# Performance work log

Measured on AMD Instinct MI355X. Metric: run time of the kernel, lower is better.

Reference implementation:

```python
import jax, jax.numpy as jnp
import numpy as np

N, E = 50000, 800000
IN_C, HID, OUT_C = 100, 128, 40
LAYERS, GROUPS, CODES = 3, 3, 16
BETA = 0.98
EPS = 1e-5


def setup_inputs() -> dict:
    key = jax.random.key(0)
    ks = jax.random.split(key, 16)
    lin = lambda k, i, o: (jax.random.normal(k, (i, o), jnp.float32) / np.sqrt(i)).astype(jnp.float32)
    d = {}
    d["x"] = jax.random.normal(ks[0], (N, IN_C), jnp.float32)
    d["src"] = jax.random.randint(ks[1], (E,), 0, N, jnp.int32)
    d["dst"] = jax.random.randint(ks[2], (E,), 0, N, jnp.int32)
    # SAGEConv params: lin_l (aggregated, with bias) and lin_r (root, no bias)
    d["W0a"], d["W0r"], d["b0"] = lin(ks[3], IN_C, HID), lin(ks[4], IN_C, HID), jnp.zeros((HID,), jnp.float32)
    d["W1a"], d["W1r"], d["b1"] = lin(ks[5], HID, HID), lin(ks[6], HID, HID), jnp.zeros((HID,), jnp.float32)
    d["W2a"], d["W2r"], d["b2"] = lin(ks[7], HID, HID), lin(ks[8], HID, HID), jnp.zeros((HID,), jnp.float32)
    # BatchNorm (eval mode: running stats) for first num_layers-1 = 2 layers
    d["bn_gamma"] = jnp.ones((2, HID), jnp.float32)
    d["bn_beta"] = jnp.zeros((2, HID), jnp.float32)
    d["bn_mean"] = jnp.zeros((2, HID), jnp.float32)
    d["bn_var"] = jnp.ones((2, HID), jnp.float32)
    # Residual VQ codebooks: [layer, group, num_codes, feature]
    d["codebooks"] = 0.1 * jax.random.normal(ks[9], (LAYERS, GROUPS, CODES, HID), jnp.float32)
    d["lin_W"] = lin(ks[10], HID, OUT_C)
    d["lin_b"] = jnp.zeros((OUT_C,), jnp.float32)
    return d


def _sage_conv(h, src, dst, Wa, Wr, b):
    # mean neighbor aggregation (PyG SAGEConv, aggr='mean')
    msg = h[src]                                              # [E, d]
    agg = jax.ops.segment_sum(msg, dst, num_segments=N)       # [N, d]
    deg = jax.ops.segment_sum(jnp.ones((E,), h.dtype), dst, num_segments=N)
    agg = agg / jnp.maximum(deg, 1.0)[:, None]
    return agg @ Wa + b + h @ Wr


def _rvq(h, cb):
    # residual vector quantization over GROUPS codebooks; cb: [G, K, D]
    res, quant, ids = h, jnp.zeros_like(h), []
    for g in range(GROUPS):
        c = cb[g]                                             # [K, D]
        d2 = (jnp.sum(res * res, -1, keepdims=True)
              - 2.0 * res @ c.T + jnp.sum(c * c, -1))          # [N, K]
        idx = jnp.argmin(d2, axis=-1)
        q = c[idx]
        quant = quant + q
        res = res - q
        ids.append(idx)
    sg = jax.lax.stop_gradient
    loss = (BETA * jnp.mean((h - sg(quant)) ** 2)
            + (1.0 - BETA) * jnp.mean((sg(h) - quant) ** 2))
    return loss, jnp.stack(ids, axis=1)                        # [N, G] int


def reference(x, src, dst, W0a, W0r, b0, W1a, W1r, b1, W2a, W2r, b2,
              bn_gamma, bn_beta, bn_mean, bn_var, codebooks, lin_W, lin_b):
    Ws = [(W0a, W0r, b0), (W1a, W1r, b1), (W2a, W2r, b2)]
    h = x
    total_loss = jnp.float32(0.0)
    id_list = []
    for i in range(LAYERS - 1):
        h = _sage_conv(h, src, dst, *Ws[i])
        h = (h - bn_mean[i]) * jax.lax.rsqrt(bn_var[i] + EPS) * bn_gamma[i] + bn_beta[i]
        h = jax.nn.relu(h)                                     # dropout: eval mode (identity)
        loss, ids = _rvq(h, codebooks[i])
        total_loss = total_loss + loss
        id_list.append(ids)
    h = _sage_conv(h, src, dst, *Ws[-1])
    loss, ids = _rvq(h, codebooks[-1])
    total_loss = total_loss + loss
    id_list.append(ids)
    out = h @ lin_W + lin_b
    return out, total_loss, jnp.concatenate(id_list, axis=1)
```

## Files before the change

kernel.cpp:

```cpp
#include <hip/hip_runtime.h>

#define NN 50000
#define HID 128
#define IN_C 100
#define OUT_C 40

__global__ __launch_bounds__(256)
void hist_kernel(const int* __restrict__ dst, int* __restrict__ deg, int E) {
    int e = blockIdx.x * 256 + threadIdx.x;
    if (e < E) atomicAdd(&deg[dst[e]], 1);
}

__global__ __launch_bounds__(256)
void chunk_sum_kernel(const int* __restrict__ deg, int* __restrict__ chunk_sums, int N) {
    __shared__ int s[256];
    const int t = threadIdx.x;
    const int i = blockIdx.x * 256 + t;
    s[t] = (i < N) ? deg[i] : 0;
    __syncthreads();
    for (int o = 128; o; o >>= 1) { if (t < o) s[t] += s[t + o]; __syncthreads(); }
    if (t == 0) chunk_sums[blockIdx.x] = s[0];
}

__global__ __launch_bounds__(256)
void chunk_scan_kernel(int* __restrict__ chunk_sums, int M) {
    __shared__ int s[256];
    const int t = threadIdx.x;
    int v = (t < M) ? chunk_sums[t] : 0;
    s[t] = v;
    __syncthreads();
    for (int o = 1; o < 256; o <<= 1) {
        int x = (t >= o) ? s[t - o] : 0;
        __syncthreads();
        s[t] += x;
        __syncthreads();
    }
    if (t < M) chunk_sums[t] = s[t] - v;
}

__global__ __launch_bounds__(256)
void chunk_apply_kernel(const int* __restrict__ deg, const int* __restrict__ chunk_sums,
                        int* __restrict__ row_start, int* __restrict__ cursor, int N) {
    __shared__ int s[256];
    const int t = threadIdx.x;
    const int i = blockIdx.x * 256 + t;
    int v = (i < N) ? deg[i] : 0;
    s[t] = v;
    __syncthreads();
    for (int o = 1; o < 256; o <<= 1) {
        int x = (t >= o) ? s[t - o] : 0;
        __syncthreads();
        s[t] += x;
        __syncthreads();
    }
    if (i < N) {
        int ex = chunk_sums[blockIdx.x] + s[t] - v;
        row_start[i] = ex;
        cursor[i] = ex;
        if (i == N - 1) row_start[N] = ex + v;
    }
}

__global__ __launch_bounds__(256)
void scatter_kernel(const int* __restrict__ src, const int* __restrict__ dst,
                    int* __restrict__ cursor, int* __restrict__ csr_src, int E) {
    int e = blockIdx.x * 256 + threadIdx.x;
    if (e < E) {
        int pos = atomicAdd(&cursor[dst[e]], 1);
        csr_src[pos] = src[e];
    }
}

__device__ __forceinline__ double2 ld2(const double* p) {
    return *(const double2*)p;
}
__device__ __forceinline__ double2 ld2(const float* p) {
    float2 v = *(const float2*)p;
    return make_double2((double)v.x, (double)v.y);
}

template<int K, bool HAS_BN, bool LAST, typename TIN>
__global__ __launch_bounds__(512, 6)
void layer_fused(const TIN* __restrict__ h_in,
                 const int* __restrict__ row_start, const int* __restrict__ csr_src,
                 const float* __restrict__ Wa, const float* __restrict__ Wr,
                 const float* __restrict__ b,
                 const float* __restrict__ gamma, const float* __restrict__ beta,
                 const float* __restrict__ mean, const float* __restrict__ var,
                 const float* __restrict__ cb,
                 double* __restrict__ h_out,
                 float* __restrict__ ids_out, int id_col0,
                 double* __restrict__ loss_part,
                 const float* __restrict__ lin_W, const float* __restrict__ lin_b,
                 float* __restrict__ out) {
    __shared__ double s_agg[8][HID];
    __shared__ double s_h[8][HID];
    __shared__ float s_cb[3 * 16 * 129];
    __shared__ float s_cc32[3][16];
    __shared__ double s_ws[8];
    const int t = threadIdx.x;
    const int w = t >> 6, lane = t & 63;
    const int n0 = blockIdx.x * 8;

    for (int idx = t; idx < 3 * 16 * 128; idx += 512)
        s_cb[(idx >> 7) * 129 + (idx & 127)] = cb[idx];

    {
        const int n = n0 + w;
        const int r0 = row_start[n], r1 = row_start[n + 1];
        const int f0 = 2 * lane;
        if (f0 < K) {
            double s0 = 0, s1 = 0, s2 = 0, s3 = 0, s4 = 0, s5 = 0, s6 = 0, s7 = 0;
            int i = r0;
            for (; i + 3 < r1; i += 4) {
                const double2 v0 = ld2(h_in + (size_t)csr_src[i] * K + f0);
                const double2 v1 = ld2(h_in + (size_t)csr_src[i + 1] * K + f0);
                const double2 v2 = ld2(h_in + (size_t)csr_src[i + 2] * K + f0);
                const double2 v3 = ld2(h_in + (size_t)csr_src[i + 3] * K + f0);
                s0 += v0.x; s1 += v0.y; s2 += v1.x; s3 += v1.y;
                s4 += v2.x; s5 += v2.y; s6 += v3.x; s7 += v3.y;
            }
            for (; i < r1; ++i) {
                const double2 v = ld2(h_in + (size_t)csr_src[i] * K + f0);
                s0 += v.x; s1 += v.y;
            }
            const int deg = r1 - r0;
            const double dd = (double)(deg > 1 ? deg : 1);
            const double2 root = ld2(h_in + (size_t)n * K + f0);
            s_agg[w][f0]     = ((s0 + s2) + (s4 + s6)) / dd;
            s_agg[w][f0 + 1] = ((s1 + s3) + (s5 + s7)) / dd;
            s_h[w][f0]     = root.x;
            s_h[w][f0 + 1] = root.y;
        }
    }
    __syncthreads();

    const int col = t & 127;
    const int p4 = t >> 7;
    double accA = (double)b[col];
    double accB = accA;
#pragma unroll 4
    for (int k = 0; k < K; ++k) {
        const double wa = (double)Wa[(size_t)k * HID + col];
        const double wr = (double)Wr[(size_t)k * HID + col];
        accA += s_agg[p4][k] * wa + s_h[p4][k] * wr;
        accB += s_agg[p4 + 4][k] * wa + s_h[p4 + 4][k] * wr;
    }
    __syncthreads();

    {
        double vA = accA, vB = accB;
        if (HAS_BN) {
            const double scale = (double)gamma[col] / sqrt((double)var[col] + 1e-5);
            const double shift = (double)beta[col] - (double)mean[col] * scale;
            vA = vA * scale + shift; vA = vA > 0.0 ? vA : 0.0;
            vB = vB * scale + shift; vB = vB > 0.0 ? vB : 0.0;
        }
        h_out[(size_t)(n0 + p4) * HID + col] = vA;
        h_out[(size_t)(n0 + p4 + 4) * HID + col] = vB;
        s_agg[p4][col] = vA;
        s_agg[p4 + 4][col] = vB;
        if (LAST) {
            s_h[p4][col] = vA;
            s_h[p4 + 4][col] = vB;
        }
    }
    if (t < 48) {
        const float* c = &s_cb[t * 129];
        double s = 0.0;
        for (int j = 0; j < 128; j++) { double cj = (double)c[j]; s += cj * cj; }
        s_cc32[t >> 4][t & 15] = (float)s;
    }
    __syncthreads();

    {
        double* res = &s_agg[w][0];
        const int n = n0 + w;
        const int k = lane & 15, q = lane >> 4;

        for (int g = 0; g < 3; ++g) {
            double r0 = res[lane], r1 = res[lane + 64];
            double pr = r0 * r0 + r1 * r1;
            pr += __shfl_xor(pr, 1, 64);
            pr += __shfl_xor(pr, 2, 64);
            pr += __shfl_xor(pr, 4, 64);
            pr += __shfl_xor(pr, 8, 64);
            pr += __shfl_xor(pr, 16, 64);
            pr += __shfl_xor(pr, 32, 64);
            const float rr32 = (float)pr;

            const float* c = &s_cb[(g * 16 + k) * 129];
            double dot = 0.0;
#pragma unroll
            for (int j2 = 0; j2 < 32; ++j2) {
                int j = q * 32 + ((j2 + q * 8) & 31);
                dot += res[j] * (double)c[j];
            }
            dot += __shfl_xor(dot, 16, 64);
            dot += __shfl_xor(dot, 32, 64);

            const float rc32 = (float)dot;
            const float t1 = rr32 - 2.0f * rc32;
            const float d2 = t1 + s_cc32[g][k];

            float bv = d2; int bk = k;
            {
                float ov; int ok;
                ov = __shfl_xor(bv, 1, 64); ok = __shfl_xor(bk, 1, 64);
                if (ov < bv || (ov == bv && ok < bk)) { bv = ov; bk = ok; }
                ov = __shfl_xor(bv, 2, 64); ok = __shfl_xor(bk, 2, 64);
                if (ov < bv || (ov == bv && ok < bk)) { bv = ov; bk = ok; }
                ov = __shfl_xor(bv, 4, 64); ok = __shfl_xor(bk, 4, 64);
                if (ov < bv || (ov == bv && ok < bk)) { bv = ov; bk = ok; }
                ov = __shfl_xor(bv, 8, 64); ok = __shfl_xor(bk, 8, 64);
                if (ov < bv || (ov == bv && ok < bk)) { bv = ov; bk = ok; }
            }
            if (lane == 0)
                ids_out[(size_t)n * 9 + id_col0 + g] = (float)bk;

            res[lane]      -= (double)s_cb[(g * 16 + bk) * 129 + lane];
            res[lane + 64] -= (double)s_cb[(g * 16 + bk) * 129 + lane + 64];
        }
        double r0 = res[lane], r1 = res[lane + 64];
        double wl = r0 * r0 + r1 * r1;
        wl += __shfl_xor(wl, 1, 64);
        wl += __shfl_xor(wl, 2, 64);
        wl += __shfl_xor(wl, 4, 64);
        wl += __shfl_xor(wl, 8, 64);
        wl += __shfl_xor(wl, 16, 64);
        wl += __shfl_xor(wl, 32, 64);
        if (lane == 0) s_ws[w] = wl;
    }

    if (LAST) {
        const int n = n0 + w;
        if (lane < OUT_C) {
            double acc = (double)lin_b[lane];
            for (int kk = 0; kk < HID; ++kk)
                acc += s_h[w][kk] * (double)lin_W[kk * OUT_C + lane];
            out[(size_t)n * OUT_C + lane] = (float)acc;
        }
    }

    __syncthreads();
    if (t == 0) {
        double s = 0.0;
#pragma unroll
        for (int i = 0; i < 8; i++) s += s_ws[i];
        loss_part[blockIdx.x] = s;
    }
}

__global__ __launch_bounds__(256)
void finalize_kernel(const double* __restrict__ loss_part, int M,
                     float* __restrict__ out_loss) {
    __shared__ double s[256];
    const int t = threadIdx.x;
    double v = 0.0;
    for (int i = t; i < M; i += 256) v += loss_part[i];
    s[t] = v;
    __syncthreads();
    for (int off = 128; off; off >>= 1) {
        if (t < off) s[t] += s[t + off];
        __syncthreads();
    }
    if (t == 0) out_loss[0] = (float)(s[0] / ((double)NN * (double)HID));
}

extern "C" void kernel_launch(void* const* d_in, const int* in_sizes, int n_in,
                              void* d_out, int out_size, void* d_ws, size_t ws_size,
                              hipStream_t stream) {
    const float* x    = (const float*)d_in[0];
    const int*   src  = (const int*)d_in[1];
    const int*   dst  = (const int*)d_in[2];
    const float* W0a = (const float*)d_in[3];
    const float* W0r = (const float*)d_in[4];
    const float* b0  = (const float*)d_in[5];
    const float* W1a = (const float*)d_in[6];
    const float* W1r = (const float*)d_in[7];
    const float* b1  = (const float*)d_in[8];
    const float* W2a = (const float*)d_in[9];
    const float* W2r = (const float*)d_in[10];
    const float* b2  = (const float*)d_in[11];
    const float* bn_gamma = (const float*)d_in[12];
    const float* bn_beta  = (const float*)d_in[13];
    const float* bn_mean  = (const float*)d_in[14];
    const float* bn_var   = (const float*)d_in[15];
    const float* cb    = (const float*)d_in[16];
    const float* lin_W = (const float*)d_in[17];
    const float* lin_b = (const float*)d_in[18];

    const int E = in_sizes[1];

    float* out      = (float*)d_out;
    float* out_loss = out + (size_t)NN * OUT_C;
    float* out_ids  = out_loss + 1;

    char* base = (char*)d_ws;
    size_t off = 0;
    auto alloc = [&](size_t bytes) -> void* {
        off = (off + 511) & ~(size_t)511;
        void* p = base + off;
        off += bytes;
        return p;
    };
    int* deg_i      = (int*)alloc((size_t)NN * 4);
    int* row_start  = (int*)alloc((size_t)(NN + 1) * 4);
    int* cursor     = (int*)alloc((size_t)NN * 4);
    int* csr_src    = (int*)alloc((size_t)E * 4);
    int* chunk_sums = (int*)alloc(256 * 4);
    double* loss_part = (double*)alloc((size_t)3 * 6250 * 8);
    double* h1 = (double*)alloc((size_t)NN * HID * 8);
    double* h2 = (double*)alloc((size_t)NN * HID * 8);

    const int cb_layer = 3 * 16 * HID;
    const int NB = NN / 8;
    const int NCHUNK = (NN + 255) / 256;

    hipMemsetAsync(deg_i, 0, NN * sizeof(int), stream);
    hist_kernel<<<(E + 255) / 256, 256, 0, stream>>>(dst, deg_i, E);
    chunk_sum_kernel<<<NCHUNK, 256, 0, stream>>>(deg_i, chunk_sums, NN);
    chunk_scan_kernel<<<1, 256, 0, stream>>>(chunk_sums, NCHUNK);
    chunk_apply_kernel<<<NCHUNK, 256, 0, stream>>>(deg_i, chunk_sums, row_start, cursor, NN);
    scatter_kernel<<<(E + 255) / 256, 256, 0, stream>>>(src, dst, cursor, csr_src, E);

    layer_fused<IN_C, true, false, float><<<NB, 512, 0, stream>>>(
        x, row_start, csr_src, W0a, W0r, b0, bn_gamma, bn_beta, bn_mean, bn_var,
        cb + 0 * cb_layer, h1, out_ids, 0, loss_part, nullptr, nullptr, nullptr);

    layer_fused<HID, true, false, double><<<NB, 512, 0, stream>>>(
        h1, row_start, csr_src, W1a, W1r, b1,
        bn_gamma + HID, bn_beta + HID, bn_mean + HID, bn_var + HID,
        cb + 1 * cb_layer, h2, out_ids, 3, loss_part + NB, nullptr, nullptr, nullptr);

    layer_fused<HID, false, true, double><<<NB, 512, 0, stream>>>(
        h2, row_start, csr_src, W2a, W2r, b2, nullptr, nullptr, nullptr, nullptr,
        cb + 2 * cb_layer, h1, out_ids, 6, loss_part + 2 * NB, lin_W, lin_b, out);

    finalize_kernel<<<1, 256, 0, stream>>>(loss_part, 3 * NB, out_loss);
}
```

Baseline: 950.2 us.

## Split neighbor aggregation into a separate high-occupancy gather kernel

The CSR mean-aggregation gather moves out of the fused layer kernel into its own lightweight kernel with 256-thread blocks, writing aggregated features to a global buffer. The remaining MLP+BN+RVQ kernel reads that buffer instead of doing the gather. The heavy fused kernel's large shared-memory and register footprint limited occupancy during the latency-bound irregular gather, and splitting it out lets more waves overlap the gather latency. The cost is an extra round trip of an N×128 double buffer per layer plus extra launches. The last layer also stops writing its unused h_out.

```diff
diff --git a/kernel.cpp b/kernel.cpp
--- a/kernel.cpp
+++ b/kernel.cpp
@@ -72,27 +72,56 @@
 }
 
 __device__ __forceinline__ double2 ld2(const double* p) {
-    return *(const double2*)p;
+    return *(const double2*)(p);
 }
 __device__ __forceinline__ double2 ld2(const float* p) {
-    float2 v = *(const float2*)p;
+    float2 v = *(const float2*)(p);
     return make_double2((double)v.x, (double)v.y);
+}
+
+template<int K, typename TIN>
+__global__ __launch_bounds__(256, 8)
+void agg_kernel(const TIN* __restrict__ h_in, const int* __restrict__ row_start,
+                const int* __restrict__ csr_src, double* __restrict__ aggout) {
+    const int t = threadIdx.x;
+    const int w = t >> 6, lane = t & 63;
+    const int n = blockIdx.x * 4 + w;
+    const int f0 = 2 * lane;
+    if (f0 >= K) return;
+    const int r0 = row_start[n], r1 = row_start[n + 1];
+    double s0 = 0, s1 = 0, s2 = 0, s3 = 0, s4 = 0, s5 = 0, s6 = 0, s7 = 0;
+    int i = r0;
+    for (; i + 3 < r1; i += 4) {
+        const double2 v0 = ld2(h_in + (size_t)csr_src[i] * K + f0);
+        const double2 v1 = ld2(h_in + (size_t)csr_src[i + 1] * K + f0);
+        const double2 v2 = ld2(h_in + (size_t)csr_src[i + 2] * K + f0);
+        const double2 v3 = ld2(h_in + (size_t)csr_src[i + 3] * K + f0);
+        s0 += v0.x; s1 += v0.y; s2 += v1.x; s3 += v1.y;
+        s4 += v2.x; s5 += v2.y; s6 += v3.x; s7 += v3.y;
+    }
+    for (; i < r1; ++i) {
+        const double2 v = ld2(h_in + (size_t)csr_src[i] * K + f0);
+        s0 += v.x; s1 += v.y;
+    }
+    const int deg = r1 - r0;
+    const double dd = (double)(deg > 1 ? deg : 1);
+    aggout[(size_t)n * HID + f0]     = ((s0 + s2) + (s4 + s6)) / dd;
+    aggout[(size_t)n * HID + f0 + 1] = ((s1 + s3) + (s5 + s7)) / dd;
 }
 
 template<int K, bool HAS_BN, bool LAST, typename TIN>
 __global__ __launch_bounds__(512, 6)
-void layer_fused(const TIN* __restrict__ h_in,
-                 const int* __restrict__ row_start, const int* __restrict__ csr_src,
-                 const float* __restrict__ Wa, const float* __restrict__ Wr,
-                 const float* __restrict__ b,
-                 const float* __restrict__ gamma, const float* __restrict__ beta,
-                 const float* __restrict__ mean, const float* __restrict__ var,
-                 const float* __restrict__ cb,
-                 double* __restrict__ h_out,
-                 float* __restrict__ ids_out, int id_col0,
-                 double* __restrict__ loss_part,
-                 const float* __restrict__ lin_W, const float* __restrict__ lin_b,
-                 float* __restrict__ out) {
+void mlp_rvq(const TIN* __restrict__ h_in, const double* __restrict__ aggin,
+             const float* __restrict__ Wa, const float* __restrict__ Wr,
+             const float* __restrict__ b,
+             const float* __restrict__ gamma, const float* __restrict__ beta,
+             const float* __restrict__ mean, const float* __restrict__ var,
+             const float* __restrict__ cb,
+             double* __restrict__ h_out,
+             float* __restrict__ ids_out, int id_col0,
+             double* __restrict__ loss_part,
+             const float* __restrict__ lin_W, const float* __restrict__ lin_b,
+             float* __restrict__ out) {
     __shared__ double s_agg[8][HID];
     __shared__ double s_h[8][HID];
     __shared__ float s_cb[3 * 16 * 129];
@@ -107,28 +136,12 @@
 
     {
         const int n = n0 + w;
-        const int r0 = row_start[n], r1 = row_start[n + 1];
         const int f0 = 2 * lane;
         if (f0 < K) {
-            double s0 = 0, s1 = 0, s2 = 0, s3 = 0, s4 = 0, s5 = 0, s6 = 0, s7 = 0;
-            int i = r0;
-            for (; i + 3 < r1; i += 4) {
-                const double2 v0 = ld2(h_in + (size_t)csr_src[i] * K + f0);
-                const double2 v1 = ld2(h_in + (size_t)csr_src[i + 1] * K + f0);
-                const double2 v2 = ld2(h_in + (size_t)csr_src[i + 2] * K + f0);
-                const double2 v3 = ld2(h_in + (size_t)csr_src[i + 3] * K + f0);
-                s0 += v0.x; s1 += v0.y; s2 += v1.x; s3 += v1.y;
-                s4 += v2.x; s5 += v2.y; s6 += v3.x; s7 += v3.y;
-            }
-            for (; i < r1; ++i) {
-                const double2 v = ld2(h_in + (size_t)csr_src[i] * K + f0);
-                s0 += v.x; s1 += v.y;
-            }
-            const int deg = r1 - r0;
-            const double dd = (double)(deg > 1 ? deg : 1);
+            const double2 a = *(const double2*)(aggin + (size_t)n * HID + f0);
             const double2 root = ld2(h_in + (size_t)n * K + f0);
-            s_agg[w][f0]     = ((s0 + s2) + (s4 + s6)) / dd;
-            s_agg[w][f0 + 1] = ((s1 + s3) + (s5 + s7)) / dd;
+            s_agg[w][f0]     = a.x;
+            s_agg[w][f0 + 1] = a.y;
             s_h[w][f0]     = root.x;
             s_h[w][f0 + 1] = root.y;
         }
@@ -156,8 +169,10 @@
             vA = vA * scale + shift; vA = vA > 0.0 ? vA : 0.0;
             vB = vB * scale + shift; vB = vB > 0.0 ? vB : 0.0;
         }
-        h_out[(size_t)(n0 + p4) * HID + col] = vA;
-        h_out[(size_t)(n0 + p4 + 4) * HID + col] = vB;
+        if (!LAST) {
+            h_out[(size_t)(n0 + p4) * HID + col] = vA;
+            h_out[(size_t)(n0 + p4 + 4) * HID + col] = vB;
+        }
         s_agg[p4][col] = vA;
         s_agg[p4 + 4][col] = vB;
         if (LAST) {
@@ -315,6 +330,7 @@
 
     const int cb_layer = 3 * 16 * HID;
     const int NB = NN / 8;
+    const int NA = NN / 4;
     const int NCHUNK = (NN + 255) / 256;
 
     hipMemsetAsync(deg_i, 0, NN * sizeof(int), stream);
@@ -324,18 +340,21 @@
     chunk_apply_kernel<<<NCHUNK, 256, 0, stream>>>(deg_i, chunk_sums, row_start, cursor, NN);
     scatter_kernel<<<(E + 255) / 256, 256, 0, stream>>>(src, dst, cursor, csr_src, E);
 
-    layer_fused<IN_C, true, false, float><<<NB, 512, 0, stream>>>(
-        x, row_start, csr_src, W0a, W0r, b0, bn_gamma, bn_beta, bn_mean, bn_var,
+    agg_kernel<IN_C, float><<<NA, 256, 0, stream>>>(x, row_start, csr_src, h1);
+    mlp_rvq<IN_C, true, false, float><<<NB, 512, 0, stream>>>(
+        x, h1, W0a, W0r, b0, bn_gamma, bn_beta, bn_mean, bn_var,
         cb + 0 * cb_layer, h1, out_ids, 0, loss_part, nullptr, nullptr, nullptr);
 
-    layer_fused<HID, true, false, double><<<NB, 512, 0, stream>>>(
-        h1, row_start, csr_src, W1a, W1r, b1,
+    agg_kernel<HID, double><<<NA, 256, 0, stream>>>(h1, row_start, csr_src, h2);
+    mlp_rvq<HID, true, false, double><<<NB, 512, 0, stream>>>(
+        h1, h2, W1a, W1r, b1,
         bn_gamma + HID, bn_beta + HID, bn_mean + HID, bn_var + HID,
         cb + 1 * cb_layer, h2, out_ids, 3, loss_part + NB, nullptr, nullptr, nullptr);
 
-    layer_fused<HID, false, true, double><<<NB, 512, 0, stream>>>(
-        h2, row_start, csr_src, W2a, W2r, b2, nullptr, nullptr, nullptr, nullptr,
-        cb + 2 * cb_layer, h1, out_ids, 6, loss_part + 2 * NB, lin_W, lin_b, out);
+    agg_kernel<HID, double><<<NA, 256, 0, stream>>>(h2, row_start, csr_src, h1);
+    mlp_rvq<HID, false, true, double><<<NB, 512, 0, stream>>>(
+        h2, h1, W2a, W2r, b2, nullptr, nullptr, nullptr, nullptr,
+        cb + 2 * cb_layer, nullptr, out_ids, 6, loss_part + 2 * NB, lin_W, lin_b, out);
 
     finalize_kernel<<<1, 256, 0, stream>>>(loss_part, 3 * NB, out_loss);
 }
```

New measurement: 1.104 ms. 16.2% more time.
